# Kernel tuning notes

Hardware: AMD Instinct MI355X
Metric: run time of the kernel (lower is better)

Reference implementation:

```python
import jax, jax.numpy as jnp
import numpy as np

B, H, W, C = 8, 64, 64, 256
RC = C // 8  # reduced channels per build()

def setup_inputs() -> dict:
    key = jax.random.key(0)
    ks = jax.random.split(key, 4)
    x = jax.random.normal(ks[0], (B, H, W, C), dtype=jnp.float32)
    # 1x1 conv kernels flattened to [Cin, Cout]; glorot-ish scale
    wq = jax.random.normal(ks[1], (C, RC), dtype=jnp.float32) * (1.0 / np.sqrt(C))
    wk = jax.random.normal(ks[2], (C, RC), dtype=jnp.float32) * (1.0 / np.sqrt(C))
    wv = jax.random.normal(ks[3], (C, C), dtype=jnp.float32) * (1.0 / np.sqrt(C))
    bq = jnp.zeros((RC,), dtype=jnp.float32)
    bk = jnp.zeros((RC,), dtype=jnp.float32)
    bv = jnp.zeros((C,), dtype=jnp.float32)
    return {"x": x, "wq": wq, "bq": bq, "wk": wk, "bk": bk, "wv": wv, "bv": bv}

def reference(x, wq, bq, wk, bk, wv, bv):
    b, h, w, c = x.shape
    n = h * w
    # 1x1 convs == per-pixel channel matmuls; q/k have relu activation, v does not
    q = jax.nn.relu(jnp.einsum('bhwc,cd->bhwd', x, wq) + bq).reshape(b, n, -1)  # [B,N,RC]
    k = jax.nn.relu(jnp.einsum('bhwc,cd->bhwd', x, wk) + bk).reshape(b, n, -1)  # [B,N,RC]
    v = (jnp.einsum('bhwc,cd->bhwd', x, wv) + bv).reshape(b, n, c)              # [B,N,C]
    attn = jax.nn.softmax(jnp.einsum('bnd,bmd->bnm', q, k), axis=-1)            # [B,N,N]
    out = jnp.einsum('bnm,bmc->bnc', attn, v).reshape(b, h, w, c)
    return out + x
```

## Files before the change

kernel.cpp:

```cpp
#include <hip/hip_runtime.h>
#include <hip/hip_bf16.h>

typedef __attribute__((ext_vector_type(8))) short s16x8;
typedef __attribute__((ext_vector_type(4))) float f32x4;
typedef __attribute__((ext_vector_type(4))) unsigned int u32x4;

#define BATCH 8
#define NPIX  4096
#define CCH   256
#define RCH   32
#define TK    32
#define HALFK 2048
#define NIT   (HALFK / TK)
#define THR   8.0f
#define LOG2E 1.4426950408889634f

__device__ __forceinline__ unsigned short f2bf(float f) {
  __hip_bfloat16 h = __float2bfloat16(f);
  return __builtin_bit_cast(unsigned short, h);
}

__device__ __forceinline__ unsigned int cvt_pk(float lo, float hi) {
  unsigned int r;
  asm("v_cvt_pk_bf16_f32 %0, %1, %2" : "=v"(r) : "v"(lo), "v"(hi));
  return r;
}

__device__ __forceinline__ void gload_lds16(const void* g, void* l) {
  __builtin_amdgcn_global_load_lds(
      (const __attribute__((address_space(1))) void*)g,
      (__attribute__((address_space(3))) void*)l, 16, 0, 0);
}

__global__ void prep_kernel(const float* __restrict__ x,
                            const float* __restrict__ wq,
                            const float* __restrict__ wk,
                            const float* __restrict__ wv,
                            unsigned short* __restrict__ xb,
                            unsigned short* __restrict__ wqkT,
                            unsigned short* __restrict__ wvT) {
  int stride = gridDim.x * blockDim.x;
  int i0 = blockIdx.x * blockDim.x + threadIdx.x;
  const int nx4 = BATCH * NPIX * CCH / 4;
  for (int i = i0; i < nx4; i += stride) {
    float4 v = reinterpret_cast<const float4*>(x)[i];
    ushort4 o;
    o.x = f2bf(v.x); o.y = f2bf(v.y); o.z = f2bf(v.z); o.w = f2bf(v.w);
    reinterpret_cast<ushort4*>(xb)[i] = o;
  }
  for (int i = i0; i < 64 * CCH; i += stride) {
    int d = i >> 8, c = i & 255;
    float v = (d < RCH) ? wq[c * RCH + d] : wk[c * RCH + (d - RCH)];
    wqkT[i] = f2bf(v);
  }
  for (int i = i0; i < CCH * CCH; i += stride) {
    int d = i >> 8, c = i & 255;
    wvT[i] = f2bf(wv[c * CCH + d]);
  }
}

__global__ void qk_proj_kernel(const unsigned short* __restrict__ xb,
                               const unsigned short* __restrict__ wqkT,
                               const float* __restrict__ bq,
                               const float* __restrict__ bk,
                               unsigned short* __restrict__ qb,
                               unsigned short* __restrict__ kb) {
  int t = threadIdx.x;
  int w = t >> 6, l = t & 63, g = l >> 4, lc = l & 15;
  int row0 = blockIdx.x * 64 + w * 16;
  f32x4 zero = {0.f, 0.f, 0.f, 0.f};
  f32x4 acc[4];
  for (int ct = 0; ct < 4; ++ct) acc[ct] = zero;
  for (int ks = 0; ks < 8; ++ks) {
    s16x8 a = *reinterpret_cast<const s16x8*>(
        xb + (size_t)(row0 + lc) * CCH + ks * 32 + g * 8);
    for (int ct = 0; ct < 4; ++ct) {
      s16x8 bfr = *reinterpret_cast<const s16x8*>(
          wqkT + (size_t)(ct * 16 + lc) * CCH + ks * 32 + g * 8);
      acc[ct] = __builtin_amdgcn_mfma_f32_16x16x32_bf16(a, bfr, acc[ct], 0, 0, 0);
    }
  }
  for (int ct = 0; ct < 4; ++ct) {
    int col = ct * 16 + lc;
    float bias = (col < RCH) ? bq[col] : bk[col - RCH];
    for (int r = 0; r < 4; ++r) {
      int row = row0 + 4 * g + r;
      float v = fmaxf(acc[ct][r] + bias, 0.f);
      if (col < RCH) qb[(size_t)row * RCH + col] = f2bf(v * LOG2E);
      else           kb[(size_t)row * RCH + (col - RCH)] = f2bf(v);
    }
  }
}

__global__ void v_proj_kernel(const unsigned short* __restrict__ xb,
                              const unsigned short* __restrict__ wvT,
                              const float* __restrict__ bv,
                              unsigned short* __restrict__ vT) {
  int t = threadIdx.x;
  int w = t >> 6, l = t & 63, g = l >> 4, lc = l & 15;
  int idx = blockIdx.x;
  int b = idx & 7; idx >>= 3;
  int dt = idx & 3; int nt = idx >> 2;
  int d0 = dt * 64 + w * 16;
  int n0 = nt * 64;
  f32x4 zero = {0.f, 0.f, 0.f, 0.f};
  f32x4 acc[4];
  for (int ct = 0; ct < 4; ++ct) acc[ct] = zero;
  for (int ks = 0; ks < 8; ++ks) {
    s16x8 a = *reinterpret_cast<const s16x8*>(
        wvT + (size_t)(d0 + lc) * CCH + ks * 32 + g * 8);
    for (int ct = 0; ct < 4; ++ct) {
      s16x8 bfr = *reinterpret_cast<const s16x8*>(
          xb + ((size_t)b * NPIX + n0 + ct * 16 + lc) * CCH + ks * 32 + g * 8);
      acc[ct] = __builtin_amdgcn_mfma_f32_16x16x32_bf16(a, bfr, acc[ct], 0, 0, 0);
    }
  }
  for (int ct = 0; ct < 4; ++ct) {
    for (int r = 0; r < 4; ++r) {
      int d = d0 + 4 * g + r;
      int n = n0 + ct * 16 + lc;
      vT[((size_t)b * CCH + d) * NPIX + n] = f2bf(acc[ct][r] + bv[d]);
    }
  }
}

__global__ __launch_bounds__(256, 2)
void attn_kernel(const unsigned short* __restrict__ qb,
                 const unsigned short* __restrict__ kb,
                 const unsigned short* __restrict__ vT,
                 const float* __restrict__ x,
                 float* __restrict__ out) {
  __shared__ __attribute__((aligned(16))) unsigned short Vlds[2][CCH * 64];
  __shared__ __attribute__((aligned(16))) float mergeLS[2][32];
  __shared__ float mLds[2];

  int b  = blockIdx.x & 7;
  int qt = blockIdx.x >> 3;
  int t  = threadIdx.x;
  int w = t >> 6, l = t & 63, g = l >> 4, lc = l & 15;
  int a = w >> 1, s = w & 1;
  const size_t bN = (size_t)b * NPIX;
  f32x4 zero = {0.f, 0.f, 0.f, 0.f};

  const unsigned short* kbase = kb + bN * RCH;
  const unsigned short* vbase = vT + (size_t)b * CCH * NPIX;

  int qbase = qt * 64 + a * 32;
  s16x8 qfA = *reinterpret_cast<const s16x8*>(qb + (bN + qbase + lc) * RCH + g * 8);
  s16x8 qfB = *reinterpret_cast<const s16x8*>(qb + (bN + qbase + 16 + lc) * RCH + g * 8);

  int chb = t >> 3, gr = t & 7;
  int gsw = gr ^ (chb & 7);
  int koff = (gsw < 4) ? (gsw * 8) : (HALFK + (gsw - 4) * 8);
  const unsigned short* vsrc = vbase + (size_t)chb * NPIX + koff;

  int krb = 8 * (lc >> 2) + (lc & 3);
  int kO  = s * HALFK + krb;

  unsigned int swz = (lc & 7) << 4;
  int vrS = (s * 64 + g * 16) ^ swz;

  s16x8 ones;
  #pragma unroll
  for (int i = 0; i < 8; ++i) ones[i] = (short)0x3F80;

  f32x4 o[2][16];
  #pragma unroll
  for (int qh = 0; qh < 2; ++qh)
    #pragma unroll
    for (int cc = 0; cc < 16; ++cc) o[qh][cc] = zero;
  f32x4 ols[2];
  ols[0] = zero; ols[1] = zero;
  float m = -1e30f;

  #pragma unroll
  for (int i = 0; i < 8; ++i)
    gload_lds16(vsrc + (size_t)i * 32 * NPIX,
                (char*)&Vlds[0][0] + i * 4096 + t * 16);
  s16x8 kf0 = *reinterpret_cast<const s16x8*>(kbase + (size_t)(kO + 0) * RCH + g * 8);
  s16x8 kf1 = *reinterpret_cast<const s16x8*>(kbase + (size_t)(kO + 4) * RCH + g * 8);
  __syncthreads();

  for (int it = 0; it < NIT; ++it) {
    int p = it & 1;
    int kv = it * TK;
    bool nx = (it + 1) < NIT;

    if (nx) {
      #pragma unroll
      for (int i = 0; i < 8; ++i)
        gload_lds16(vsrc + kv + TK + (size_t)i * 32 * NPIX,
                    (char*)&Vlds[p ^ 1][0] + i * 4096 + t * 16);
    }

    f32x4 sA0 = __builtin_amdgcn_mfma_f32_16x16x32_bf16(kf0, qfA, zero, 0, 0, 0);
    f32x4 sA1 = __builtin_amdgcn_mfma_f32_16x16x32_bf16(kf1, qfA, zero, 0, 0, 0);
    f32x4 sB0 = __builtin_amdgcn_mfma_f32_16x16x32_bf16(kf0, qfB, zero, 0, 0, 0);
    f32x4 sB1 = __builtin_amdgcn_mfma_f32_16x16x32_bf16(kf1, qfB, zero, 0, 0, 0);

    if (nx) {
      kf0 = *reinterpret_cast<const s16x8*>(
          kbase + (size_t)(kO + kv + TK + 0) * RCH + g * 8);
      kf1 = *reinterpret_cast<const s16x8*>(
          kbase + (size_t)(kO + kv + TK + 4) * RCH + g * 8);
    }

    float xA = fmaxf(fmaxf(sA0[0], sA0[1]), fmaxf(sA0[2], sA0[3]));
    float xB = fmaxf(fmaxf(sA1[0], sA1[1]), fmaxf(sA1[2], sA1[3]));
    float xC = fmaxf(fmaxf(sB0[0], sB0[1]), fmaxf(sB0[2], sB0[3]));
    float xD = fmaxf(fmaxf(sB1[0], sB1[1]), fmaxf(sB1[2], sB1[3]));
    float pmax = fmaxf(fmaxf(xA, xB), fmaxf(xC, xD));

    float sc = 1.f;
    int resc = !__all(pmax - m <= THR);
    if (resc) {
      #pragma unroll
      for (int off = 1; off <= 32; off <<= 1)
        pmax = fmaxf(pmax, __shfl_xor(pmax, off));
      float mnew = fmaxf(m, pmax);
      sc = exp2f(m - mnew);
      m = mnew;
    }

    unsigned int pkA[4], pkB[4];
    pkA[0] = cvt_pk(exp2f(sA0[0] - m), exp2f(sA0[1] - m));
    pkA[1] = cvt_pk(exp2f(sA0[2] - m), exp2f(sA0[3] - m));
    pkA[2] = cvt_pk(exp2f(sA1[0] - m), exp2f(sA1[1] - m));
    pkA[3] = cvt_pk(exp2f(sA1[2] - m), exp2f(sA1[3] - m));
    pkB[0] = cvt_pk(exp2f(sB0[0] - m), exp2f(sB0[1] - m));
    pkB[1] = cvt_pk(exp2f(sB0[2] - m), exp2f(sB0[3] - m));
    pkB[2] = cvt_pk(exp2f(sB1[0] - m), exp2f(sB1[1] - m));
    pkB[3] = cvt_pk(exp2f(sB1[2] - m), exp2f(sB1[3] - m));

    if (resc) {
      #pragma unroll
      for (int qh = 0; qh < 2; ++qh) {
        #pragma unroll
        for (int cc = 0; cc < 16; ++cc)
          #pragma unroll
          for (int r = 0; r < 4; ++r) o[qh][cc][r] *= sc;
        #pragma unroll
        for (int r = 0; r < 4; ++r) ols[qh][r] *= sc;
      }
    }

    u32x4 uA = {pkA[0], pkA[1], pkA[2], pkA[3]};
    u32x4 uB = {pkB[0], pkB[1], pkB[2], pkB[3]};
    s16x8 paA = __builtin_bit_cast(s16x8, uA);
    s16x8 paB = __builtin_bit_cast(s16x8, uB);
    const char* pb = (const char*)&Vlds[p][0] + lc * 128 + vrS;
    __builtin_amdgcn_s_setprio(1);
    ols[0] = __builtin_amdgcn_mfma_f32_16x16x32_bf16(paA, ones, ols[0], 0, 0, 0);
    ols[1] = __builtin_amdgcn_mfma_f32_16x16x32_bf16(paB, ones, ols[1], 0, 0, 0);
    #pragma unroll
    for (int cc = 0; cc < 16; ++cc) {
      s16x8 vb = *reinterpret_cast<const s16x8*>(pb + cc * 2048);
      o[0][cc] = __builtin_amdgcn_mfma_f32_16x16x32_bf16(paA, vb, o[0][cc], 0, 0, 0);
      o[1][cc] = __builtin_amdgcn_mfma_f32_16x16x32_bf16(paB, vb, o[1][cc], 0, 0, 0);
    }
    __builtin_amdgcn_s_setprio(0);

    __syncthreads();
  }

  if (s == 1) {
    if (lc == 0) {
      *reinterpret_cast<f32x4*>(&mergeLS[a][4 * g])      = ols[0];
      *reinterpret_cast<f32x4*>(&mergeLS[a][16 + 4 * g]) = ols[1];
    }
    if (l == 0) mLds[a] = m;
  }
  __syncthreads();

  float* mrg = (float*)&Vlds[0][0];
  if (s == 1) {
    float* base = mrg + a * 8192 + l * 128;
    #pragma unroll
    for (int qh = 0; qh < 2; ++qh)
      #pragma unroll
      for (int cc = 0; cc < 16; ++cc) {
        int idx = qh * 16 + cc;
        *reinterpret_cast<f32x4*>(base + ((idx + l) & 31) * 4) = o[qh][cc];
      }
  }
  __syncthreads();
  if (s == 0) {
    float mB = mLds[a];
    float mT = fmaxf(m, mB);
    float sAc = exp2f(m - mT), sBc = exp2f(mB - mT);
    const float* base = mrg + a * 8192 + l * 128;
    #pragma unroll
    for (int qh = 0; qh < 2; ++qh) {
      f32x4 lB4 = *reinterpret_cast<const f32x4*>(&mergeLS[a][qh * 16 + 4 * g]);
      f32x4 rl;
      #pragma unroll
      for (int r = 0; r < 4; ++r)
        rl[r] = 1.0f / (ols[qh][r] * sAc + lB4[r] * sBc);
      #pragma unroll
      for (int cc = 0; cc < 16; ++cc) {
        int idx = qh * 16 + cc;
        f32x4 ob = *reinterpret_cast<const f32x4*>(base + ((idx + l) & 31) * 4);
        #pragma unroll
        for (int r = 0; r < 4; ++r) {
          size_t row = bN + qbase + qh * 16 + 4 * g + r;
          size_t oi = row * CCH + cc * 16 + lc;
          out[oi] = (o[qh][cc][r] * sAc + ob[r] * sBc) * rl[r] + x[oi];
        }
      }
    }
  }
}

extern "C" void kernel_launch(void* const* d_in, const int* in_sizes, int n_in,
                              void* d_out, int out_size, void* d_ws, size_t ws_size,
                              hipStream_t stream) {
  const float* x  = (const float*)d_in[0];
  const float* wq = (const float*)d_in[1];
  const float* bq = (const float*)d_in[2];
  const float* wk = (const float*)d_in[3];
  const float* bk = (const float*)d_in[4];
  const float* wv = (const float*)d_in[5];
  const float* bv = (const float*)d_in[6];
  float* out = (float*)d_out;

  unsigned short* ws   = (unsigned short*)d_ws;
  unsigned short* qb   = ws;
  unsigned short* kb   = qb + 1048576;
  unsigned short* vT   = kb + 1048576;
  unsigned short* xb   = vT + 8388608;
  unsigned short* wqkT = xb + 8388608;
  unsigned short* wvT  = wqkT + 16384;

  prep_kernel<<<dim3(2048), dim3(256), 0, stream>>>(x, wq, wk, wv, xb, wqkT, wvT);
  qk_proj_kernel<<<dim3(512), dim3(256), 0, stream>>>(xb, wqkT, bq, bk, qb, kb);
  v_proj_kernel<<<dim3(2048), dim3(256), 0, stream>>>(xb, wvT, bv, vT);
  attn_kernel<<<dim3(512), dim3(256), 0, stream>>>(qb, kb, vT, x, out);
}
```

Before: 166.2 us.

## Merge projection kernels, register-stage V loads, fold max subtraction into MFMA

The Q/K and V projection kernels become one launch of 2560 blocks, removing a kernel boundary. In attention, V tiles are no longer copied with global_load_lds. They are loaded into registers and written to the other LDS buffer after the PV MFMAs, with one barrier placed mid-iteration in place of the end-of-loop syncthreads. The running max is folded into the QK MFMA accumulator init (mneg), so the per-element subtraction before exp2 goes away. This costs more VGPRs for the staged loads and changes the barrier ordering, which raises the risk of LDS hazards.

Result: no change. 166.6 us (+0.3%).

```diff
diff --git a/kernel.cpp b/kernel.cpp
--- a/kernel.cpp
+++ b/kernel.cpp
@@ -24,12 +24,6 @@
   unsigned int r;
   asm("v_cvt_pk_bf16_f32 %0, %1, %2" : "=v"(r) : "v"(lo), "v"(hi));
   return r;
-}
-
-__device__ __forceinline__ void gload_lds16(const void* g, void* l) {
-  __builtin_amdgcn_global_load_lds(
-      (const __attribute__((address_space(1))) void*)g,
-      (__attribute__((address_space(3))) void*)l, 16, 0, 0);
 }
 
 __global__ void prep_kernel(const float* __restrict__ x,
@@ -59,67 +53,65 @@
   }
 }
 
-__global__ void qk_proj_kernel(const unsigned short* __restrict__ xb,
-                               const unsigned short* __restrict__ wqkT,
-                               const float* __restrict__ bq,
-                               const float* __restrict__ bk,
-                               unsigned short* __restrict__ qb,
-                               unsigned short* __restrict__ kb) {
+__global__ void proj_kernel(const unsigned short* __restrict__ xb,
+                            const unsigned short* __restrict__ wqkT,
+                            const unsigned short* __restrict__ wvT,
+                            const float* __restrict__ bq,
+                            const float* __restrict__ bk,
+                            const float* __restrict__ bv,
+                            unsigned short* __restrict__ qb,
+                            unsigned short* __restrict__ kb,
+                            unsigned short* __restrict__ vT) {
   int t = threadIdx.x;
   int w = t >> 6, l = t & 63, g = l >> 4, lc = l & 15;
-  int row0 = blockIdx.x * 64 + w * 16;
   f32x4 zero = {0.f, 0.f, 0.f, 0.f};
-  f32x4 acc[4];
-  for (int ct = 0; ct < 4; ++ct) acc[ct] = zero;
-  for (int ks = 0; ks < 8; ++ks) {
-    s16x8 a = *reinterpret_cast<const s16x8*>(
-        xb + (size_t)(row0 + lc) * CCH + ks * 32 + g * 8);
+
+  if (blockIdx.x < 512) {
+    int row0 = blockIdx.x * 64 + w * 16;
+    f32x4 acc[4];
+    for (int ct = 0; ct < 4; ++ct) acc[ct] = zero;
+    for (int ks = 0; ks < 8; ++ks) {
+      s16x8 a = *reinterpret_cast<const s16x8*>(
+          xb + (size_t)(row0 + lc) * CCH + ks * 32 + g * 8);
+      for (int ct = 0; ct < 4; ++ct) {
+        s16x8 bfr = *reinterpret_cast<const s16x8*>(
+            wqkT + (size_t)(ct * 16 + lc) * CCH + ks * 32 + g * 8);
+        acc[ct] = __builtin_amdgcn_mfma_f32_16x16x32_bf16(a, bfr, acc[ct], 0, 0, 0);
+      }
+    }
     for (int ct = 0; ct < 4; ++ct) {
-      s16x8 bfr = *reinterpret_cast<const s16x8*>(
-          wqkT + (size_t)(ct * 16 + lc) * CCH + ks * 32 + g * 8);
-      acc[ct] = __builtin_amdgcn_mfma_f32_16x16x32_bf16(a, bfr, acc[ct], 0, 0, 0);
-    }
-  }
-  for (int ct = 0; ct < 4; ++ct) {
-    int col = ct * 16 + lc;
-    float bias = (col < RCH) ? bq[col] : bk[col - RCH];
-    for (int r = 0; r < 4; ++r) {
-      int row = row0 + 4 * g + r;
-      float v = fmaxf(acc[ct][r] + bias, 0.f);
-      if (col < RCH) qb[(size_t)row * RCH + col] = f2bf(v * LOG2E);
-      else           kb[(size_t)row * RCH + (col - RCH)] = f2bf(v);
-    }
-  }
-}
-
-__global__ void v_proj_kernel(const unsigned short* __restrict__ xb,
-                              const unsigned short* __restrict__ wvT,
-                              const float* __restrict__ bv,
-                              unsigned short* __restrict__ vT) {
-  int t = threadIdx.x;
-  int w = t >> 6, l = t & 63, g = l >> 4, lc = l & 15;
-  int idx = blockIdx.x;
-  int b = idx & 7; idx >>= 3;
-  int dt = idx & 3; int nt = idx >> 2;
-  int d0 = dt * 64 + w * 16;
-  int n0 = nt * 64;
-  f32x4 zero = {0.f, 0.f, 0.f, 0.f};
-  f32x4 acc[4];
-  for (int ct = 0; ct < 4; ++ct) acc[ct] = zero;
-  for (int ks = 0; ks < 8; ++ks) {
-    s16x8 a = *reinterpret_cast<const s16x8*>(
-        wvT + (size_t)(d0 + lc) * CCH + ks * 32 + g * 8);
+      int col = ct * 16 + lc;
+      float bias = (col < RCH) ? bq[col] : bk[col - RCH];
+      for (int r = 0; r < 4; ++r) {
+        int row = row0 + 4 * g + r;
+        float v = fmaxf(acc[ct][r] + bias, 0.f);
+        if (col < RCH) qb[(size_t)row * RCH + col] = f2bf(v * LOG2E);
+        else           kb[(size_t)row * RCH + (col - RCH)] = f2bf(v);
+      }
+    }
+  } else {
+    int idx = blockIdx.x - 512;
+    int b = idx & 7; idx >>= 3;
+    int dt = idx & 3; int nt = idx >> 2;
+    int d0 = dt * 64 + w * 16;
+    int n0 = nt * 64;
+    f32x4 acc[4];
+    for (int ct = 0; ct < 4; ++ct) acc[ct] = zero;
+    for (int ks = 0; ks < 8; ++ks) {
+      s16x8 a = *reinterpret_cast<const s16x8*>(
+          wvT + (size_t)(d0 + lc) * CCH + ks * 32 + g * 8);
+      for (int ct = 0; ct < 4; ++ct) {
+        s16x8 bfr = *reinterpret_cast<const s16x8*>(
+            xb + ((size_t)b * NPIX + n0 + ct * 16 + lc) * CCH + ks * 32 + g * 8);
+        acc[ct] = __builtin_amdgcn_mfma_f32_16x16x32_bf16(a, bfr, acc[ct], 0, 0, 0);
+      }
+    }
     for (int ct = 0; ct < 4; ++ct) {
-      s16x8 bfr = *reinterpret_cast<const s16x8*>(
-          xb + ((size_t)b * NPIX + n0 + ct * 16 + lc) * CCH + ks * 32 + g * 8);
-      acc[ct] = __builtin_amdgcn_mfma_f32_16x16x32_bf16(a, bfr, acc[ct], 0, 0, 0);
-    }
-  }
-  for (int ct = 0; ct < 4; ++ct) {
-    for (int r = 0; r < 4; ++r) {
-      int d = d0 + 4 * g + r;
-      int n = n0 + ct * 16 + lc;
-      vT[((size_t)b * CCH + d) * NPIX + n] = f2bf(acc[ct][r] + bv[d]);
+      for (int r = 0; r < 4; ++r) {
+        int d = d0 + 4 * g + r;
+        int n = n0 + ct * 16 + lc;
+        vT[((size_t)b * CCH + d) * NPIX + n] = f2bf(acc[ct][r] + bv[d]);
+      }
     }
   }
 }
@@ -171,15 +163,18 @@
     for (int cc = 0; cc < 16; ++cc) o[qh][cc] = zero;
   f32x4 ols[2];
   ols[0] = zero; ols[1] = zero;
-  float m = -1e30f;
-
+  float m = 0.f;
+  f32x4 mneg = zero;
+
+  s16x8 gv[8];
   #pragma unroll
   for (int i = 0; i < 8; ++i)
-    gload_lds16(vsrc + (size_t)i * 32 * NPIX,
-                (char*)&Vlds[0][0] + i * 4096 + t * 16);
+    gv[i] = *reinterpret_cast<const s16x8*>(vsrc + (size_t)i * 32 * NPIX);
   s16x8 kf0 = *reinterpret_cast<const s16x8*>(kbase + (size_t)(kO + 0) * RCH + g * 8);
   s16x8 kf1 = *reinterpret_cast<const s16x8*>(kbase + (size_t)(kO + 4) * RCH + g * 8);
-  __syncthreads();
+  #pragma unroll
+  for (int i = 0; i < 8; ++i)
+    *reinterpret_cast<s16x8*>((char*)&Vlds[0][0] + i * 4096 + t * 16) = gv[i];
 
   for (int it = 0; it < NIT; ++it) {
     int p = it & 1;
@@ -189,14 +184,14 @@
     if (nx) {
       #pragma unroll
       for (int i = 0; i < 8; ++i)
-        gload_lds16(vsrc + kv + TK + (size_t)i * 32 * NPIX,
-                    (char*)&Vlds[p ^ 1][0] + i * 4096 + t * 16);
-    }
-
-    f32x4 sA0 = __builtin_amdgcn_mfma_f32_16x16x32_bf16(kf0, qfA, zero, 0, 0, 0);
-    f32x4 sA1 = __builtin_amdgcn_mfma_f32_16x16x32_bf16(kf1, qfA, zero, 0, 0, 0);
-    f32x4 sB0 = __builtin_amdgcn_mfma_f32_16x16x32_bf16(kf0, qfB, zero, 0, 0, 0);
-    f32x4 sB1 = __builtin_amdgcn_mfma_f32_16x16x32_bf16(kf1, qfB, zero, 0, 0, 0);
+        gv[i] = *reinterpret_cast<const s16x8*>(
+            vsrc + kv + TK + (size_t)i * 32 * NPIX);
+    }
+
+    f32x4 sA0 = __builtin_amdgcn_mfma_f32_16x16x32_bf16(kf0, qfA, mneg, 0, 0, 0);
+    f32x4 sA1 = __builtin_amdgcn_mfma_f32_16x16x32_bf16(kf1, qfA, mneg, 0, 0, 0);
+    f32x4 sB0 = __builtin_amdgcn_mfma_f32_16x16x32_bf16(kf0, qfB, mneg, 0, 0, 0);
+    f32x4 sB1 = __builtin_amdgcn_mfma_f32_16x16x32_bf16(kf1, qfB, mneg, 0, 0, 0);
 
     if (nx) {
       kf0 = *reinterpret_cast<const s16x8*>(
@@ -212,27 +207,17 @@
     float pmax = fmaxf(fmaxf(xA, xB), fmaxf(xC, xD));
 
     float sc = 1.f;
-    int resc = !__all(pmax - m <= THR);
+    int resc = !__all(pmax <= THR);
     if (resc) {
       #pragma unroll
       for (int off = 1; off <= 32; off <<= 1)
         pmax = fmaxf(pmax, __shfl_xor(pmax, off));
-      float mnew = fmaxf(m, pmax);
-      sc = exp2f(m - mnew);
-      m = mnew;
-    }
-
-    unsigned int pkA[4], pkB[4];
-    pkA[0] = cvt_pk(exp2f(sA0[0] - m), exp2f(sA0[1] - m));
-    pkA[1] = cvt_pk(exp2f(sA0[2] - m), exp2f(sA0[3] - m));
-    pkA[2] = cvt_pk(exp2f(sA1[0] - m), exp2f(sA1[1] - m));
-    pkA[3] = cvt_pk(exp2f(sA1[2] - m), exp2f(sA1[3] - m));
-    pkB[0] = cvt_pk(exp2f(sB0[0] - m), exp2f(sB0[1] - m));
-    pkB[1] = cvt_pk(exp2f(sB0[2] - m), exp2f(sB0[3] - m));
-    pkB[2] = cvt_pk(exp2f(sB1[0] - m), exp2f(sB1[1] - m));
-    pkB[3] = cvt_pk(exp2f(sB1[2] - m), exp2f(sB1[3] - m));
-
-    if (resc) {
+      float delta = fmaxf(pmax, 0.f);
+      sc = exp2f(-delta);
+      m += delta;
+      f32x4 dd = {delta, delta, delta, delta};
+      mneg -= dd;
+      sA0 -= dd; sA1 -= dd; sB0 -= dd; sB1 -= dd;
       #pragma unroll
       for (int qh = 0; qh < 2; ++qh) {
         #pragma unroll
@@ -244,14 +229,29 @@
       }
     }
 
+    unsigned int pkA[4], pkB[4];
+    pkA[0] = cvt_pk(exp2f(sA0[0]), exp2f(sA0[1]));
+    pkA[1] = cvt_pk(exp2f(sA0[2]), exp2f(sA0[3]));
+    pkA[2] = cvt_pk(exp2f(sA1[0]), exp2f(sA1[1]));
+    pkA[3] = cvt_pk(exp2f(sA1[2]), exp2f(sA1[3]));
+    pkB[0] = cvt_pk(exp2f(sB0[0]), exp2f(sB0[1]));
+    pkB[1] = cvt_pk(exp2f(sB0[2]), exp2f(sB0[3]));
+    pkB[2] = cvt_pk(exp2f(sB1[0]), exp2f(sB1[1]));
+    pkB[3] = cvt_pk(exp2f(sB1[2]), exp2f(sB1[3]));
+
     u32x4 uA = {pkA[0], pkA[1], pkA[2], pkA[3]};
     u32x4 uB = {pkB[0], pkB[1], pkB[2], pkB[3]};
     s16x8 paA = __builtin_bit_cast(s16x8, uA);
     s16x8 paB = __builtin_bit_cast(s16x8, uB);
+    ols[0] = __builtin_amdgcn_mfma_f32_16x16x32_bf16(paA, ones, ols[0], 0, 0, 0);
+    ols[1] = __builtin_amdgcn_mfma_f32_16x16x32_bf16(paB, ones, ols[1], 0, 0, 0);
+
+    asm volatile("s_waitcnt lgkmcnt(0)" ::: "memory");
+    __builtin_amdgcn_s_barrier();
+    asm volatile("" ::: "memory");
+
     const char* pb = (const char*)&Vlds[p][0] + lc * 128 + vrS;
     __builtin_amdgcn_s_setprio(1);
-    ols[0] = __builtin_amdgcn_mfma_f32_16x16x32_bf16(paA, ones, ols[0], 0, 0, 0);
-    ols[1] = __builtin_amdgcn_mfma_f32_16x16x32_bf16(paB, ones, ols[1], 0, 0, 0);
     #pragma unroll
     for (int cc = 0; cc < 16; ++cc) {
       s16x8 vb = *reinterpret_cast<const s16x8*>(pb + cc * 2048);
@@ -260,7 +260,11 @@
     }
     __builtin_amdgcn_s_setprio(0);
 
-    __syncthreads();
+    if (nx) {
+      #pragma unroll
+      for (int i = 0; i < 8; ++i)
+        *reinterpret_cast<s16x8*>((char*)&Vlds[p ^ 1][0] + i * 4096 + t * 16) = gv[i];
+    }
   }
 
   if (s == 1) {
@@ -332,7 +336,7 @@
   unsigned short* wvT  = wqkT + 16384;
 
   prep_kernel<<<dim3(2048), dim3(256), 0, stream>>>(x, wq, wk, wv, xb, wqkT, wvT);
-  qk_proj_kernel<<<dim3(512), dim3(256), 0, stream>>>(xb, wqkT, bq, bk, qb, kb);
-  v_proj_kernel<<<dim3(2048), dim3(256), 0, stream>>>(xb, wvT, bv, vT);
+  proj_kernel<<<dim3(2560), dim3(256), 0, stream>>>(xb, wqkT, wvT, bq, bk, bv,
+                                                    qb, kb, vT);
   attn_kernel<<<dim3(512), dim3(256), 0, stream>>>(qb, kb, vT, x, out);
 }
```
